# Kernel tuning notes

Measured on AMD Instinct MI355X. Metric: run time of the kernel, lower is better.

## Reference

```python
import jax, jax.numpy as jnp
import numpy as np

D_MODEL = 1024
NUM_HEADS = 16
HEAD_DIM = D_MODEL // NUM_HEADS
THETA = 10000.0
BATCH = 2
SEQ = 2048


def _apply_rope(x, positions):
    # x: (b, h, s, hd), positions: (b, s) int
    hd = x.shape[-1]
    inv_freq = 1.0 / (THETA ** (jnp.arange(0, hd, 2, dtype=jnp.float32) / hd))  # (hd/2,)
    ang = positions.astype(jnp.float32)[:, None, :, None] * inv_freq  # (b,1,s,hd/2)
    cos, sin = jnp.cos(ang), jnp.sin(ang)
    x1 = x[..., 0::2]
    x2 = x[..., 1::2]
    r1 = x1 * cos - x2 * sin
    r2 = x1 * sin + x2 * cos
    return jnp.stack([r1, r2], axis=-1).reshape(x.shape)


def setup_inputs() -> dict:
    key = jax.random.key(0)
    ks = jax.random.split(key, 5)
    scale = 1.0 / np.sqrt(D_MODEL)
    x = jax.random.normal(ks[0], (BATCH, SEQ, D_MODEL), dtype=jnp.float32)
    token_positions = jnp.broadcast_to(jnp.arange(SEQ, dtype=jnp.int32), (BATCH, SEQ))
    W_q = jax.random.normal(ks[1], (D_MODEL, D_MODEL), dtype=jnp.float32) * scale
    W_k = jax.random.normal(ks[2], (D_MODEL, D_MODEL), dtype=jnp.float32) * scale
    W_v = jax.random.normal(ks[3], (D_MODEL, D_MODEL), dtype=jnp.float32) * scale
    W_o = jax.random.normal(ks[4], (D_MODEL, D_MODEL), dtype=jnp.float32) * scale
    return {"x": x, "token_positions": token_positions, "W_q": W_q, "W_k": W_k, "W_v": W_v, "W_o": W_o}


def reference(x, token_positions, W_q, W_k, W_v, W_o):
    b, s, _ = x.shape
    h, hd = NUM_HEADS, HEAD_DIM
    # bias-free Linear: y = x @ W^T, W: (out, in)
    def proj(W):
        return jnp.einsum('bsd,ed->bse', x, W).reshape(b, s, h, hd).transpose(0, 2, 1, 3)
    Q = _apply_rope(proj(W_q), token_positions)
    K = _apply_rope(proj(W_k), token_positions)
    V = proj(W_v)
    scores = jnp.einsum('bhqd,bhkd->bhqk', Q, K) / jnp.sqrt(jnp.float32(hd))
    causal = jnp.triu(jnp.full((s, s), -jnp.inf, dtype=scores.dtype), k=1)
    attn = jax.nn.softmax(scores + causal, axis=-1)
    Z = jnp.einsum('bhqk,bhkd->bhqd', attn, V)
    Z = Z.transpose(0, 2, 1, 3).reshape(b, s, h * hd)
    return jnp.einsum('bse,de->bsd', Z, W_o)
```

## Files before the change

kernel.cpp:

```cpp
#include <hip/hip_runtime.h>
#include <hip/hip_bf16.h>


#define BATCH 2
#define SEQ   2048
#define NH    16
#define HD    64
#define DM    1024
#define MTOT  (BATCH*SEQ)

typedef __attribute__((ext_vector_type(8))) short bf16x8;
typedef __attribute__((ext_vector_type(4))) float f32x4;
typedef __attribute__((ext_vector_type(4))) unsigned int u32x4;
typedef unsigned short u16;
typedef unsigned int   u32;

__device__ __forceinline__ float b2f(u16 h){ return __uint_as_float(((u32)h) << 16); }
__device__ __forceinline__ u16 f2b(float f){
  u32 u = __float_as_uint(f);
  u32 r = (u + 0x7FFFu + ((u >> 16) & 1u)) >> 16;
  return (u16)r;
}
__device__ __forceinline__ u16 cvt1(float f){
  __hip_bfloat16 h = __float2bfloat16(f);
  return *reinterpret_cast<u16*>(&h);
}
__device__ __forceinline__ u32 pk2(float lo, float hi){
  return (u32)cvt1(lo) | ((u32)cvt1(hi) << 16);
}
__device__ __forceinline__ f32x4 mfma16(bf16x8 a, bf16x8 b, f32x4 c){
  return __builtin_amdgcn_mfma_f32_16x16x32_bf16(a, b, c, 0, 0, 0);
}
__device__ __forceinline__ void gload_lds16(const u16* g, u16* l){
  __builtin_amdgcn_global_load_lds((const __attribute__((address_space(1))) unsigned int*)g,
                                   (__attribute__((address_space(3))) unsigned int*)l, 16, 0, 0);
}

__global__ __launch_bounds__(256) void cvt_all(const float* __restrict__ x,
    const float* __restrict__ wq, const float* __restrict__ wk,
    const float* __restrict__ wv, const float* __restrict__ wo,
    u16* __restrict__ xb, u16* __restrict__ wb)
{
  const long NX = (long)MTOT * DM;
  const long NW = (long)DM * DM;
  const long tot4 = (NX + 4*NW) >> 2;
  for (long t = (long)blockIdx.x*blockDim.x + threadIdx.x; t < tot4;
       t += (long)gridDim.x*blockDim.x){
    long e = t << 2;
    const float* s; u16* d;
    if (e < NX){ s = x + e; d = xb + e; }
    else {
      long j = e - NX; int z = (int)(j >> 20);
      const float* ws = (z==0)?wq:(z==1)?wk:(z==2)?wv:wo;
      s = ws + (j & (NW-1)); d = wb + j;
    }
    float4 v = *(const float4*)s;
    u32 lo = (u32)f2b(v.x) | ((u32)f2b(v.y) << 16);
    u32 hi = (u32)f2b(v.z) | ((u32)f2b(v.w) << 16);
    uint2 o; o.x = lo; o.y = hi;
    *(uint2*)d = o;
  }
}

__global__ __launch_bounds__(256) void rope_table(float2* __restrict__ tab){
  int t = blockIdx.x*blockDim.x + threadIdx.x;
  if (t >= SEQ*32) return;
  int s = t >> 5, i = t & 31;
  float inv = 1.0f / powf(10000.0f, (float)i * (1.0f/32.0f));
  float a = (float)s * inv;
  tab[t] = make_float2(cosf(a), sinf(a));
}

__device__ __forceinline__ void gemm128_core(const u16* __restrict__ A, const u16* __restrict__ B,
    int mbase, int nbase, u16* Alds, u16* Blds, f32x4 acc[4][4])
{
  const int tid = threadIdx.x;
  const int w = tid >> 6, l = tid & 63, g = l >> 4, c = l & 15;
  const int wr = (w >> 1)*64, wc = (w & 1)*64;
  const int srow = l >> 3;
  const int scol = ((l & 7) ^ srow)*8;
  const u16* Ag = A + (long)(mbase + w*32 + srow)*DM + scol;
  const u16* Bg = B + (long)(nbase + w*32 + srow)*DM + scol;
  u16* Alb = Alds + w*2048;
  u16* Blb = Blds + w*2048;

  for (int k0 = 0; k0 < DM; k0 += 64){
    __syncthreads();
    #pragma unroll
    for (int i = 0; i < 4; i++){
      gload_lds16(Ag + k0 + (long)(8*i)*DM, Alb + i*512);
      gload_lds16(Bg + k0 + (long)(8*i)*DM, Blb + i*512);
    }
    __syncthreads();
    #pragma unroll
    for (int ks = 0; ks < 2; ks++){
      bf16x8 af[4], bfr[4];
      #pragma unroll
      for (int mi = 0; mi < 4; mi++){
        int row = wr + mi*16 + c;
        af[mi] = *(const bf16x8*)&Alds[row*64 + (((ks*4 + g) ^ (row & 7))*8)];
      }
      #pragma unroll
      for (int nj = 0; nj < 4; nj++){
        int row = wc + nj*16 + c;
        bfr[nj] = *(const bf16x8*)&Blds[row*64 + (((ks*4 + g) ^ (row & 7))*8)];
      }
      #pragma unroll
      for (int mi = 0; mi < 4; mi++)
        #pragma unroll
        for (int nj = 0; nj < 4; nj++)
          acc[mi][nj] = mfma16(af[mi], bfr[nj], acc[mi][nj]);
    }
  }
}

__global__ __launch_bounds__(256) void gemm_qkv(const u16* __restrict__ xb,
                                                const u16* __restrict__ wb,
                                                u16* __restrict__ qkvr)
{
  __shared__ u16 Alds[128*64];
  __shared__ u16 Blds[128*64];
  const int z = blockIdx.z;
  const u16* Bm = wb + (long)z * DM * DM;
  u16* C = qkvr + (long)z * MTOT * DM;
  const int nbase = blockIdx.x*128, mbase = blockIdx.y*128;
  const int w = threadIdx.x >> 6, l = threadIdx.x & 63, g = l >> 4, c = l & 15;
  const int wr = (w >> 1)*64, wc = (w & 1)*64;
  f32x4 acc[4][4] = {};
  gemm128_core(xb, Bm, mbase, nbase, Alds, Blds, acc);
  #pragma unroll
  for (int mi = 0; mi < 4; mi++)
    #pragma unroll
    for (int nj = 0; nj < 4; nj++)
      #pragma unroll
      for (int r = 0; r < 4; r++){
        int row = mbase + wr + mi*16 + 4*g + r;
        int col = nbase + wc + nj*16 + c;
        C[(long)row*DM + col] = f2b(acc[mi][nj][r]);
      }
}

__global__ __launch_bounds__(256) void gemm_out(const u16* __restrict__ Zb,
                                                const u16* __restrict__ wob,
                                                float* __restrict__ out)
{
  __shared__ u16 Alds[128*64];
  __shared__ u16 Blds[64*64];
  const int nbase = blockIdx.x*64, mbase = blockIdx.y*128;
  const int tid = threadIdx.x;
  const int w = tid >> 6, l = tid & 63, g = l >> 4, c = l & 15;
  const int wr = (w >> 1)*64, wc = (w & 1)*32;
  const int srow = l >> 3;
  const int scol = ((l & 7) ^ srow)*8;
  const u16* Ag = Zb  + (long)(mbase + w*32 + srow)*DM + scol;
  const u16* Bg = wob + (long)(nbase + w*16 + srow)*DM + scol;
  u16* Alb = Alds + w*2048;
  u16* Blb = Blds + w*1024;
  f32x4 acc[4][2] = {};

  for (int k0 = 0; k0 < DM; k0 += 64){
    __syncthreads();
    #pragma unroll
    for (int i = 0; i < 4; i++)
      gload_lds16(Ag + k0 + (long)(8*i)*DM, Alb + i*512);
    #pragma unroll
    for (int i = 0; i < 2; i++)
      gload_lds16(Bg + k0 + (long)(8*i)*DM, Blb + i*512);
    __syncthreads();
    #pragma unroll
    for (int ks = 0; ks < 2; ks++){
      bf16x8 af[4], bfr[2];
      #pragma unroll
      for (int mi = 0; mi < 4; mi++){
        int row = wr + mi*16 + c;
        af[mi] = *(const bf16x8*)&Alds[row*64 + (((ks*4 + g) ^ (row & 7))*8)];
      }
      #pragma unroll
      for (int nj = 0; nj < 2; nj++){
        int row = wc + nj*16 + c;
        bfr[nj] = *(const bf16x8*)&Blds[row*64 + (((ks*4 + g) ^ (row & 7))*8)];
      }
      #pragma unroll
      for (int mi = 0; mi < 4; mi++)
        #pragma unroll
        for (int nj = 0; nj < 2; nj++)
          acc[mi][nj] = mfma16(af[mi], bfr[nj], acc[mi][nj]);
    }
  }
  #pragma unroll
  for (int mi = 0; mi < 4; mi++)
    #pragma unroll
    for (int nj = 0; nj < 2; nj++)
      #pragma unroll
      for (int r = 0; r < 4; r++){
        int row = mbase + wr + mi*16 + 4*g + r;
        int col = nbase + wc + nj*16 + c;
        out[(long)row*DM + col] = acc[mi][nj][r];
      }
}

__global__ __launch_bounds__(256) void rope_scatter(const u16* __restrict__ qkvr,
    u16* __restrict__ Qd, u16* __restrict__ Kd, u16* __restrict__ Vt,
    const float2* __restrict__ tab, const int* __restrict__ pos)
{
  int st = blockIdx.x, h = blockIdx.y, b = blockIdx.z;
  int s0 = st*64;
  const u16* Qraw = qkvr;
  const u16* Kraw = qkvr + (long)MTOT*DM;
  const u16* Vraw = qkvr + 2L*MTOT*DM;
  const float SC = 0.125f * 1.44269504089f;

  for (int t = threadIdx.x; t < 64*32; t += 256){
    int sl = t >> 5, i = t & 31;
    int s = s0 + sl;
    int p = pos[b*SEQ + s];
    if (p < 0) p = 0; if (p >= SEQ) p = SEQ - 1;
    float2 cs = tab[p*32 + i];
    long inoff  = (long)(b*SEQ + s)*DM + h*HD + 2*i;
    long outoff = ((long)(b*NH + h)*SEQ + s)*HD + 2*i;
    u32 qe = *(const u32*)(Qraw + inoff);
    float x1 = b2f((u16)(qe & 0xffff)), x2 = b2f((u16)(qe >> 16));
    float r1 = (x1*cs.x - x2*cs.y)*SC;
    float r2 = (x1*cs.y + x2*cs.x)*SC;
    *(u32*)(Qd + outoff) = (u32)f2b(r1) | ((u32)f2b(r2) << 16);
    u32 ke = *(const u32*)(Kraw + inoff);
    x1 = b2f((u16)(ke & 0xffff)); x2 = b2f((u16)(ke >> 16));
    r1 = x1*cs.x - x2*cs.y;
    r2 = x1*cs.y + x2*cs.x;
    *(u32*)(Kd + outoff) = (u32)f2b(r1) | ((u32)f2b(r2) << 16);
  }

  __shared__ u16 vt[64][65];
  for (int t = threadIdx.x; t < 64*8; t += 256){
    int sl = t >> 3, ch = (t & 7)*8;
    bf16x8 v = *(const bf16x8*)(Vraw + (long)(b*SEQ + s0 + sl)*DM + h*HD + ch);
    #pragma unroll
    for (int j = 0; j < 8; j++) vt[sl][ch + j] = (u16)v[j];
  }
  __syncthreads();
  for (int t = threadIdx.x; t < 64*8; t += 256){
    int d = t >> 3, ch = (t & 7)*8;
    bf16x8 v;
    #pragma unroll
    for (int j = 0; j < 8; j++) v[j] = (short)vt[ch + j][d];
    *(bf16x8*)(Vt + ((long)(b*NH + h)*HD + d)*SEQ + s0 + ch) = v;
  }
}

__device__ __forceinline__ int kperm(int a){
  return (a & 32) | ((a & 4) << 2) | ((a & 24) >> 1) | (a & 3);
}

__global__ __launch_bounds__(256) void attn(const u16* __restrict__ Q, const u16* __restrict__ K,
                                            const u16* __restrict__ Vt,
                                            u16* __restrict__ Opart, float* __restrict__ Lsum)
{
  const int pair = (int)blockIdx.x >> 1;
  const int half = blockIdx.x & 1;
  const int h = blockIdx.y, b = blockIdx.z;
  const int tid = threadIdx.x, w = tid >> 6, l = tid & 63, g = l >> 4, c = l & 15;
  const u16* Kp = K  + (long)(b*NH + h)*SEQ*HD;
  const u16* Vp = Vt + (long)(b*NH + h)*HD*SEQ;

  __shared__ u16 KV[2][2][64][64];
  u16* kv = &KV[0][0][0][0];

  const int srow0 = tid >> 3, sch = tid & 7;
  const int kpr0 = kperm(srow0), kpr1 = kperm(srow0 + 32);
  const int cswz = c & 7;

  const int wk0 = kpr0*64 + (sch ^ (kpr0 & 7))*8;
  const int wk1 = kpr1*64 + (sch ^ (kpr1 & 7))*8;
  const int wv0 = 4096 + srow0*64 + (sch ^ (srow0 & 7))*8;
  const int wv1 = 4096 + (srow0 + 32)*64 + (sch ^ ((srow0 + 32) & 7))*8;
  const int ra0 = c*64 + (((0 + g) ^ cswz)*8);
  const int ra1 = c*64 + (((4 + g) ^ cswz)*8);

  bf16x8 ones;
  #pragma unroll
  for (int j = 0; j < 8; j++) ones[j] = (short)0x3F80;

  int bufo = 0;
  #pragma unroll 1
  for (int seg = 0; seg < 2; ++seg){
    const int qt = seg ? (31 - pair) : pair;
    const int qbase = qt*64;
    const int qrow = qbase + w*16;
    const u16* Qp = Q + ((long)(b*NH + h)*SEQ + qrow)*HD;
    bf16x8 qf0 = *(const bf16x8*)(Qp + c*HD + g*8);
    bf16x8 qf1 = *(const bf16x8*)(Qp + c*HD + 32 + g*8);

    const int ntH0  = (qt + 2) >> 1;
    const int tstart = half ? ntH0 : 0;
    const int tend   = half ? (qt + 1) : ntH0;

    f32x4 accz[4] = {};
    f32x4 lacc = {};

    if (tstart < tend){
      __syncthreads();
      const u16* kg0 = Kp + (long)(tstart*64 + srow0)*HD + sch*8;
      const u16* kg1 = kg0 + 32*HD;
      const u16* vg0 = Vp + (long)srow0*SEQ + tstart*64 + sch*8;
      const u16* vg1 = vg0 + 32*SEQ;
      bf16x8 kr0 = *(const bf16x8*)kg0, kr1 = *(const bf16x8*)kg1;
      bf16x8 vr0 = *(const bf16x8*)vg0, vr1 = *(const bf16x8*)vg1;
      kg0 += 64*HD; kg1 += 64*HD; vg0 += 64; vg1 += 64;
      *(bf16x8*)(kv + bufo + wk0) = kr0;
      *(bf16x8*)(kv + bufo + wk1) = kr1;
      *(bf16x8*)(kv + bufo + wv0) = vr0;
      *(bf16x8*)(kv + bufo + wv1) = vr1;

      for (int t = tstart; t < tend; ++t){
        const int kbase = t*64;
        __syncthreads();

        if (t < tend-1){
          kr0 = *(const bf16x8*)kg0; kr1 = *(const bf16x8*)kg1;
          vr0 = *(const bf16x8*)vg0; vr1 = *(const bf16x8*)vg1;
          kg0 += 64*HD; kg1 += 64*HD; vg0 += 64; vg1 += 64;
        }

        const u16* kvb = kv + bufo;

        f32x4 s[4];
        __builtin_amdgcn_s_setprio(1);
        #pragma unroll
        for (int sub = 0; sub < 4; sub++){
          bf16x8 ka0 = *(const bf16x8*)(kvb + ra0 + sub*1024);
          bf16x8 ka1 = *(const bf16x8*)(kvb + ra1 + sub*1024);
          f32x4 z4 = {};
          z4 = mfma16(ka0, qf0, z4);
          z4 = mfma16(ka1, qf1, z4);
          s[sub] = z4;
        }
        __builtin_amdgcn_s_setprio(0);

        const bool edge = (kbase + 63 > qrow);
        const int q = qrow + c;
        if (edge){
          #pragma unroll
          for (int sub = 0; sub < 4; sub++)
            #pragma unroll
            for (int r = 0; r < 4; r++){
              int key = kbase + ((sub >> 1) << 5) + 8*g + ((sub & 1) << 2) + r;
              if (key > q) s[sub][r] = -1e30f;
            }
        }
        #pragma unroll
        for (int sub = 0; sub < 4; sub++)
          #pragma unroll
          for (int r = 0; r < 4; r++)
            s[sub][r] = exp2f(s[sub][r]);

        u32x4 p0, p1;
        p0[0] = pk2(s[0][0], s[0][1]); p0[1] = pk2(s[0][2], s[0][3]);
        p0[2] = pk2(s[1][0], s[1][1]); p0[3] = pk2(s[1][2], s[1][3]);
        p1[0] = pk2(s[2][0], s[2][1]); p1[1] = pk2(s[2][2], s[2][3]);
        p1[2] = pk2(s[3][0], s[3][1]); p1[3] = pk2(s[3][2], s[3][3]);
        bf16x8 pf0 = __builtin_bit_cast(bf16x8, p0);
        bf16x8 pf1 = __builtin_bit_cast(bf16x8, p1);

        __builtin_amdgcn_s_setprio(1);
        lacc = mfma16(pf0, ones, lacc);
        lacc = mfma16(pf1, ones, lacc);
        #pragma unroll
        for (int dt = 0; dt < 4; dt++){
          bf16x8 vf0 = *(const bf16x8*)(kvb + 4096 + ra0 + dt*1024);
          bf16x8 vf1 = *(const bf16x8*)(kvb + 4096 + ra1 + dt*1024);
          accz[dt] = mfma16(pf0, vf0, accz[dt]);
          accz[dt] = mfma16(pf1, vf1, accz[dt]);
        }
        __builtin_amdgcn_s_setprio(0);

        if (t < tend-1){
          int nbo = bufo ^ 8192;
          *(bf16x8*)(kv + nbo + wk0) = kr0;
          *(bf16x8*)(kv + nbo + wk1) = kr1;
          *(bf16x8*)(kv + nbo + wv0) = vr0;
          *(bf16x8*)(kv + nbo + wv1) = vr1;
          bufo = nbo;
        }
      }
    }

    const int pbase = (((b*NH + h)*32 + qt)*2 + half);
    if (c == 0){
      #pragma unroll
      for (int r = 0; r < 4; r++)
        Lsum[pbase*64 + w*16 + 4*g + r] = lacc[r];
    }
    u16* Op = Opart + (long)pbase*(64*64);
    #pragma unroll
    for (int dt = 0; dt < 4; dt++)
      #pragma unroll
      for (int r = 0; r < 4; r++)
        Op[(w*16 + 4*g + r)*64 + dt*16 + c] = cvt1(accz[dt][r]);
  }
}

__global__ __launch_bounds__(256) void attn_combine(const u16* __restrict__ Opart,
                                                    const float* __restrict__ Lsum,
                                                    u16* __restrict__ Z)
{
  const int qt = blockIdx.x, h = blockIdx.y, b = blockIdx.z;
  const int p0 = ((b*NH + h)*32 + qt)*2, p1 = p0 + 1;
  const int row = threadIdx.x >> 2;
  const int d0  = (threadIdx.x & 3)*16;
  float inv = 1.f / (Lsum[p0*64 + row] + Lsum[p1*64 + row]);
  const u16* o0 = Opart + ((long)p0*64 + row)*64 + d0;
  const u16* o1 = Opart + ((long)p1*64 + row)*64 + d0;
  const int s = qt*64 + row;
  u16* zp = Z + (long)(b*SEQ + s)*DM + h*HD + d0;
  #pragma unroll
  for (int j = 0; j < 2; j++){
    bf16x8 va = *(const bf16x8*)(o0 + j*8);
    bf16x8 vb = *(const bf16x8*)(o1 + j*8);
    bf16x8 ov;
    #pragma unroll
    for (int e = 0; e < 8; e++){
      float z = (b2f((u16)va[e]) + b2f((u16)vb[e]))*inv;
      ov[e] = (short)cvt1(z);
    }
    *(bf16x8*)(zp + j*8) = ov;
  }
}

extern "C" void kernel_launch(void* const* d_in, const int* in_sizes, int n_in,
                              void* d_out, int out_size, void* d_ws, size_t ws_size,
                              hipStream_t stream)
{
  const float* x  = (const float*)d_in[0];
  const int*   pos= (const int*)d_in[1];
  const float* wq = (const float*)d_in[2];
  const float* wk = (const float*)d_in[3];
  const float* wv = (const float*)d_in[4];
  const float* wo = (const float*)d_in[5];
  float* out = (float*)d_out;

  const long NX = (long)MTOT*DM;
  const long NW = (long)DM*DM;
  char* p = (char*)d_ws;
  u16* xb   = (u16*)p;  p += NX*2;
  u16* wb   = (u16*)p;  p += 4*NW*2;
  u16* qkvr = (u16*)p;  p += 3*NX*2;
  u16* Qd   = (u16*)p;  p += NX*2;
  u16* Kd   = (u16*)p;  p += NX*2;
  u16* Vt   = (u16*)p;  p += NX*2;
  u16* Zb   = (u16*)p;  p += NX*2;
  float2* tab = (float2*)p; p += (long)SEQ*32*sizeof(float2);
  u16* Opart = (u16*)p;  p += 2L*NX*2;
  float* Lsum = (float*)p; p += 2048L*64*sizeof(float);
  (void)ws_size; (void)n_in; (void)in_sizes; (void)out_size;

  hipLaunchKernelGGL(cvt_all,     dim3(2048),      dim3(256), 0, stream, x, wq, wk, wv, wo, xb, wb);
  hipLaunchKernelGGL(rope_table,  dim3(256),       dim3(256), 0, stream, tab);
  hipLaunchKernelGGL(gemm_qkv,    dim3(8,32,3),    dim3(256), 0, stream, xb, wb, qkvr);
  hipLaunchKernelGGL(rope_scatter,dim3(32,16,2),   dim3(256), 0, stream, qkvr, Qd, Kd, Vt, tab, pos);
  hipLaunchKernelGGL(attn,        dim3(32,16,2),   dim3(256), 0, stream, Qd, Kd, Vt, Opart, Lsum);
  hipLaunchKernelGGL(attn_combine,dim3(32,16,2),   dim3(256), 0, stream, Opart, Lsum, Zb);
  hipLaunchKernelGGL(gemm_out,    dim3(16,32),     dim3(256), 0, stream, Zb, wb + 3*NW, out);
}
```

Measured before the change: 119.7 us.

## Fuse RoPE, scaling and V transpose into QKV GEMM epilogue

Drops the separate rope_scatter kernel and the qkvr intermediate buffer. The QKV GEMM epilogue now applies RoPE, using a lane shuffle to fetch the paired column, and writes Q and K directly in head-major layout. It also writes V transposed as 4-element vectors along the sequence axis. This saves a kernel launch and a full round trip of the three projections through global memory. In exchange, the epilogue stores become narrow scattered writes (2-byte for Q/K, 8-byte strided for V), and it does extra table and position loads.

```diff
diff --git a/kernel.cpp b/kernel.cpp
--- a/kernel.cpp
+++ b/kernel.cpp
@@ -71,18 +71,28 @@
   tab[t] = make_float2(cosf(a), sinf(a));
 }
 
-__device__ __forceinline__ void gemm128_core(const u16* __restrict__ A, const u16* __restrict__ B,
-    int mbase, int nbase, u16* Alds, u16* Blds, f32x4 acc[4][4])
-{
+__global__ __launch_bounds__(256) void gemm_qkv(const u16* __restrict__ xb,
+                                                const u16* __restrict__ wb,
+                                                u16* __restrict__ Qd, u16* __restrict__ Kd,
+                                                u16* __restrict__ Vt,
+                                                const float2* __restrict__ tab,
+                                                const int* __restrict__ pos)
+{
+  __shared__ u16 Alds[128*64];
+  __shared__ u16 Blds[128*64];
+  const int z = blockIdx.z;
+  const u16* Bm = wb + (long)z * DM * DM;
+  const int nbase = blockIdx.x*128, mbase = blockIdx.y*128;
   const int tid = threadIdx.x;
   const int w = tid >> 6, l = tid & 63, g = l >> 4, c = l & 15;
   const int wr = (w >> 1)*64, wc = (w & 1)*64;
   const int srow = l >> 3;
   const int scol = ((l & 7) ^ srow)*8;
-  const u16* Ag = A + (long)(mbase + w*32 + srow)*DM + scol;
-  const u16* Bg = B + (long)(nbase + w*32 + srow)*DM + scol;
+  const u16* Ag = xb + (long)(mbase + w*32 + srow)*DM + scol;
+  const u16* Bg = Bm + (long)(nbase + w*32 + srow)*DM + scol;
   u16* Alb = Alds + w*2048;
   u16* Blb = Blds + w*2048;
+  f32x4 acc[4][4] = {};
 
   for (int k0 = 0; k0 < DM; k0 += 64){
     __syncthreads();
@@ -112,32 +122,48 @@
           acc[mi][nj] = mfma16(af[mi], bfr[nj], acc[mi][nj]);
     }
   }
-}
-
-__global__ __launch_bounds__(256) void gemm_qkv(const u16* __restrict__ xb,
-                                                const u16* __restrict__ wb,
-                                                u16* __restrict__ qkvr)
-{
-  __shared__ u16 Alds[128*64];
-  __shared__ u16 Blds[128*64];
-  const int z = blockIdx.z;
-  const u16* Bm = wb + (long)z * DM * DM;
-  u16* C = qkvr + (long)z * MTOT * DM;
-  const int nbase = blockIdx.x*128, mbase = blockIdx.y*128;
-  const int w = threadIdx.x >> 6, l = threadIdx.x & 63, g = l >> 4, c = l & 15;
-  const int wr = (w >> 1)*64, wc = (w & 1)*64;
-  f32x4 acc[4][4] = {};
-  gemm128_core(xb, Bm, mbase, nbase, Alds, Blds, acc);
-  #pragma unroll
-  for (int mi = 0; mi < 4; mi++)
-    #pragma unroll
-    for (int nj = 0; nj < 4; nj++)
+
+  if (z == 2){
+    #pragma unroll
+    for (int mi = 0; mi < 4; mi++){
+      int row0 = mbase + wr + mi*16 + 4*g;
+      int bb = row0 >> 11, s0 = row0 & (SEQ-1);
+      #pragma unroll
+      for (int nj = 0; nj < 4; nj++){
+        int col = nbase + wc + nj*16 + c;
+        int hh = col >> 6, d = col & 63;
+        ushort4 v;
+        v.x = cvt1(acc[mi][nj][0]); v.y = cvt1(acc[mi][nj][1]);
+        v.z = cvt1(acc[mi][nj][2]); v.w = cvt1(acc[mi][nj][3]);
+        *(ushort4*)&Vt[((long)(bb*NH + hh)*HD + d)*SEQ + s0] = v;
+      }
+    }
+  } else {
+    u16* Out = (z == 0) ? Qd : Kd;
+    const float scale = (z == 0) ? 0.125f*1.44269504089f : 1.f;
+    const bool even = (c & 1) == 0;
+    #pragma unroll
+    for (int mi = 0; mi < 4; mi++){
       #pragma unroll
       for (int r = 0; r < 4; r++){
         int row = mbase + wr + mi*16 + 4*g + r;
-        int col = nbase + wc + nj*16 + c;
-        C[(long)row*DM + col] = f2b(acc[mi][nj][r]);
-      }
+        int bb = row >> 11, s = row & (SEQ-1);
+        int p = pos[bb*SEQ + s];
+        if (p < 0) p = 0; if (p >= SEQ) p = SEQ - 1;
+        #pragma unroll
+        for (int nj = 0; nj < 4; nj++){
+          int col = nbase + wc + nj*16 + c;
+          float2 cs = tab[p*32 + ((col & 63) >> 1)];
+          float own = acc[mi][nj][r];
+          float prt = __shfl_xor(own, 1);
+          float rr = even ? (own*cs.x - prt*cs.y) : (prt*cs.y + own*cs.x);
+          rr *= scale;
+          int hh = col >> 6, d = col & 63;
+          Out[((long)(bb*NH + hh)*SEQ + s)*HD + d] = cvt1(rr);
+        }
+      }
+    }
+  }
 }
 
 __global__ __launch_bounds__(256) void gemm_out(const u16* __restrict__ Zb,
@@ -197,54 +223,6 @@
         int col = nbase + wc + nj*16 + c;
         out[(long)row*DM + col] = acc[mi][nj][r];
       }
-}
-
-__global__ __launch_bounds__(256) void rope_scatter(const u16* __restrict__ qkvr,
-    u16* __restrict__ Qd, u16* __restrict__ Kd, u16* __restrict__ Vt,
-    const float2* __restrict__ tab, const int* __restrict__ pos)
-{
-  int st = blockIdx.x, h = blockIdx.y, b = blockIdx.z;
-  int s0 = st*64;
-  const u16* Qraw = qkvr;
-  const u16* Kraw = qkvr + (long)MTOT*DM;
-  const u16* Vraw = qkvr + 2L*MTOT*DM;
-  const float SC = 0.125f * 1.44269504089f;
-
-  for (int t = threadIdx.x; t < 64*32; t += 256){
-    int sl = t >> 5, i = t & 31;
-    int s = s0 + sl;
-    int p = pos[b*SEQ + s];
-    if (p < 0) p = 0; if (p >= SEQ) p = SEQ - 1;
-    float2 cs = tab[p*32 + i];
-    long inoff  = (long)(b*SEQ + s)*DM + h*HD + 2*i;
-    long outoff = ((long)(b*NH + h)*SEQ + s)*HD + 2*i;
-    u32 qe = *(const u32*)(Qraw + inoff);
-    float x1 = b2f((u16)(qe & 0xffff)), x2 = b2f((u16)(qe >> 16));
-    float r1 = (x1*cs.x - x2*cs.y)*SC;
-    float r2 = (x1*cs.y + x2*cs.x)*SC;
-    *(u32*)(Qd + outoff) = (u32)f2b(r1) | ((u32)f2b(r2) << 16);
-    u32 ke = *(const u32*)(Kraw + inoff);
-    x1 = b2f((u16)(ke & 0xffff)); x2 = b2f((u16)(ke >> 16));
-    r1 = x1*cs.x - x2*cs.y;
-    r2 = x1*cs.y + x2*cs.x;
-    *(u32*)(Kd + outoff) = (u32)f2b(r1) | ((u32)f2b(r2) << 16);
-  }
-
-  __shared__ u16 vt[64][65];
-  for (int t = threadIdx.x; t < 64*8; t += 256){
-    int sl = t >> 3, ch = (t & 7)*8;
-    bf16x8 v = *(const bf16x8*)(Vraw + (long)(b*SEQ + s0 + sl)*DM + h*HD + ch);
-    #pragma unroll
-    for (int j = 0; j < 8; j++) vt[sl][ch + j] = (u16)v[j];
-  }
-  __syncthreads();
-  for (int t = threadIdx.x; t < 64*8; t += 256){
-    int d = t >> 3, ch = (t & 7)*8;
-    bf16x8 v;
-    #pragma unroll
-    for (int j = 0; j < 8; j++) v[j] = (short)vt[ch + j][d];
-    *(bf16x8*)(Vt + ((long)(b*NH + h)*HD + d)*SEQ + s0 + ch) = v;
-  }
 }
 
 __device__ __forceinline__ int kperm(int a){
@@ -443,7 +421,6 @@
   char* p = (char*)d_ws;
   u16* xb   = (u16*)p;  p += NX*2;
   u16* wb   = (u16*)p;  p += 4*NW*2;
-  u16* qkvr = (u16*)p;  p += 3*NX*2;
   u16* Qd   = (u16*)p;  p += NX*2;
   u16* Kd   = (u16*)p;  p += NX*2;
   u16* Vt   = (u16*)p;  p += NX*2;
@@ -455,8 +432,7 @@
 
   hipLaunchKernelGGL(cvt_all,     dim3(2048),      dim3(256), 0, stream, x, wq, wk, wv, wo, xb, wb);
   hipLaunchKernelGGL(rope_table,  dim3(256),       dim3(256), 0, stream, tab);
-  hipLaunchKernelGGL(gemm_qkv,    dim3(8,32,3),    dim3(256), 0, stream, xb, wb, qkvr);
-  hipLaunchKernelGGL(rope_scatter,dim3(32,16,2),   dim3(256), 0, stream, qkvr, Qd, Kd, Vt, tab, pos);
+  hipLaunchKernelGGL(gemm_qkv,    dim3(8,32,3),    dim3(256), 0, stream, xb, wb, Qd, Kd, Vt, tab, pos);
   hipLaunchKernelGGL(attn,        dim3(32,16,2),   dim3(256), 0, stream, Qd, Kd, Vt, Opart, Lsum);
   hipLaunchKernelGGL(attn_combine,dim3(32,16,2),   dim3(256), 0, stream, Opart, Lsum, Zb);
   hipLaunchKernelGGL(gemm_out,    dim3(16,32),     dim3(256), 0, stream, Zb, wb + 3*NW, out);
```

Measured after the change: 120.7 us. About the same (+0.8%).
